# Optimization experiments

Hardware: AMD Instinct MI355X
Metric: run time of the kernel (lower is better)

Reference implementation:

```python
import jax, jax.numpy as jnp
import numpy as np

B, T, C = 4, 4096, 1024
H, CS = 16, 128
D = C // H
EPS = 1e-5

def _ln(x, g, b):
    m = jnp.mean(x, axis=-1, keepdims=True)
    v = jnp.var(x, axis=-1, keepdims=True)
    return (x - m) * jax.lax.rsqrt(v + EPS) * g + b

def setup_inputs() -> dict:
    key = jax.random.key(0)
    ks = jax.random.split(key, 12)
    s_c = 1.0 / np.sqrt(C)
    s_2d = 1.0 / np.sqrt(2 * D)
    return {
        "x": jax.random.normal(ks[0], (B, T, C), jnp.float32),
        "mark_W": jax.random.normal(ks[1], (C, C), jnp.float32) * s_c,
        "mark_b": jnp.zeros((C,), jnp.float32),
        "gate_W": jax.random.normal(ks[2], (C, C), jnp.float32) * s_c,
        "gate_b": jnp.zeros((C,), jnp.float32),
        "carry_g": jnp.ones((D,), jnp.float32),
        "carry_b": jnp.zeros((D,), jnp.float32),
        "card_g": jnp.ones((D,), jnp.float32),
        "card_b": jnp.zeros((D,), jnp.float32),
        "ho1_W": jax.random.normal(ks[3], (2 * D, 2 * D), jnp.float32) * s_2d,
        "ho1_b": jnp.zeros((2 * D,), jnp.float32),
        "ho2_W": jax.random.normal(ks[4], (2 * D, D), jnp.float32) * s_2d,
        "ho2_b": jnp.zeros((D,), jnp.float32),
        "proj_W": jax.random.normal(ks[5], (C, C), jnp.float32) * s_c * 0.02,
        "proj_b": jnp.zeros((C,), jnp.float32),
        "ln_g": jnp.ones((C,), jnp.float32),
        "ln_b": jnp.zeros((C,), jnp.float32),
    }

def reference(x, mark_W, mark_b, gate_W, gate_b, carry_g, carry_b,
              card_g, card_b, ho1_W, ho1_b, ho2_W, ho2_b,
              proj_W, proj_b, ln_g, ln_b):
    b, t, c = x.shape
    nc = t // CS  # T chosen divisible by chunk_size -> pad_len = 0
    pm = x @ mark_W + mark_b                       # [B,T,C]
    gates = jax.nn.sigmoid(x @ gate_W + gate_b)    # [B,T,C]

    def chunks(a):  # [B,T,C] -> [B,H,nc,CS,D]
        return a.reshape(b, nc, CS, H, D).transpose(0, 3, 1, 2, 4)

    x_h = chunks(x)
    gm = chunks(gates) * chunks(pm)                # gated marks
    lcm = jnp.cumsum(gm, axis=3)                   # local prefix sum within chunk
    chunk_sums = lcm[:, :, :, -1, :]               # [B,H,nc,D]
    carry_cum = jnp.cumsum(chunk_sums, axis=2)
    carries = jnp.concatenate(
        [jnp.zeros((b, H, 1, D), x.dtype), carry_cum[:, :, :-1, :]], axis=2)
    nrm_carry = _ln(carries, carry_g, carry_b)[:, :, :, None, :]  # [B,H,nc,1,D]
    mwc = lcm + nrm_carry                          # marks with carry
    cards_local = jnp.concatenate([nrm_carry, mwc[:, :, :, :-1, :]], axis=3)
    cards = _ln(cards_local, card_g, card_b)
    comb = jnp.concatenate([x_h, cards], axis=-1)  # [B,H,nc,CS,2D]
    h = jax.nn.gelu(comb @ ho1_W + ho1_b, approximate=False)
    ho = h @ ho2_W + ho2_b                         # [B,H,nc,CS,D]
    out = ho.transpose(0, 2, 3, 1, 4).reshape(b, t, c)
    out = out @ proj_W + proj_b
    out = _ln(out, ln_g, ln_b)
    return x + out
```

## Files before the change

### kernel.cpp

```cpp
#include <hip/hip_runtime.h>
#include <hip/hip_bf16.h>

typedef __bf16 bf16_t;
typedef __attribute__((ext_vector_type(8))) __bf16 bf16x8;
typedef __attribute__((ext_vector_type(4))) __bf16 bf16x4;
typedef __attribute__((ext_vector_type(4))) float f32x4;

static constexpr int Bn = 4, Tn = 4096, Cn = 1024, Hn = 16, CSn = 128, Dn = 64, NCn = 32;

#define DEVINL __device__ __forceinline__

DEVINL float wsum64(float v) {
  v += __shfl_xor(v, 32, 64);
  v += __shfl_xor(v, 16, 64);
  v += __shfl_xor(v, 8, 64);
  v += __shfl_xor(v, 4, 64);
  v += __shfl_xor(v, 2, 64);
  v += __shfl_xor(v, 1, 64);
  return v;
}

DEVINL float gelu_f(float v) {
  float x = v * 0.70710678f;
  float ax = fabsf(x);
  float t = 1.f / (1.f + 0.3275911f * ax);
  float poly = t * (0.254829592f +
               t * (-0.284496736f +
               t * (1.421413741f +
               t * (-1.453152027f +
               t * 1.061405429f))));
  float e = __expf(-ax * ax);
  float erfax = 1.f - poly * e;
  float erfx = copysignf(erfax, x);
  return 0.5f * v * (1.f + erfx);
}

DEVINL void gld16(const bf16_t* g, bf16_t* l) {
  __builtin_amdgcn_global_load_lds(
      (const __attribute__((address_space(1))) unsigned int*)(g),
      (__attribute__((address_space(3))) unsigned int*)(l), 16, 0, 0);
}

__global__ __launch_bounds__(256) void k_xbf(const float* __restrict__ in,
                                             bf16_t* __restrict__ out) {
  int i = blockIdx.x * 256 + threadIdx.x;
  float4 a = *reinterpret_cast<const float4*>(in + (size_t)i * 8);
  float4 b = *reinterpret_cast<const float4*>(in + (size_t)i * 8 + 4);
  bf16x8 o = {(bf16_t)a.x, (bf16_t)a.y, (bf16_t)a.z, (bf16_t)a.w,
              (bf16_t)b.x, (bf16_t)b.y, (bf16_t)b.z, (bf16_t)b.w};
  *reinterpret_cast<bf16x8*>(out + (size_t)i * 8) = o;
}

__global__ void k_transpose(const float* __restrict__ in, bf16_t* __restrict__ out,
                            int rows, int cols) {
  __shared__ float tile[64][65];
  int c0 = blockIdx.x * 64, r0 = blockIdx.y * 64;
  int tx = threadIdx.x & 63, ty = threadIdx.x >> 6;
#pragma unroll
  for (int i = ty; i < 64; i += 4)
    tile[i][tx] = in[(size_t)(r0 + i) * cols + c0 + tx];
  __syncthreads();
#pragma unroll
  for (int i = ty; i < 64; i += 4)
    out[(size_t)(c0 + i) * rows + r0 + tx] = (bf16_t)tile[tx][i];
}

__global__ __launch_bounds__(256, 3) void k_dualgemm_gm(
    const bf16_t* __restrict__ X, const bf16_t* __restrict__ Wtm,
    const bf16_t* __restrict__ Wtg, const float* __restrict__ bm,
    const float* __restrict__ bg, bf16_t* __restrict__ lcm,
    float* __restrict__ csum) {
  constexpr int K = Cn, N = Cn;
  constexpr int GP = 68;
  __shared__ __align__(16) bf16_t L[16384];
  __shared__ float tot[4][64];
  int tid = threadIdx.x;
  int Lb = blockIdx.x;
  int xcd = Lb & 7, jj = Lb >> 3;
  int nb = jj & 15, mb = xcd + 8 * (jj >> 4);
  int m0 = mb * 128, n0 = nb * 64;
  int wave = tid >> 6, lane = tid & 63;
  int wm = wave >> 1, wn = wave & 1;
  int lr = lane & 15, lk = lane >> 4;
  int rl = lane >> 2;
  int cl = (lane & 3) * 8;
  f32x4 accP[4][2] = {};
  f32x4 accG[4][2] = {};

  const bf16_t* Xb = X + (size_t)m0 * K;
  const bf16_t* Wmb = Wtm + (size_t)n0 * K;
  const bf16_t* Wgb = Wtg + (size_t)n0 * K;
  bf16_t* LA = L;
  bf16_t* LBm = L + 8192;
  bf16_t* LBg = L + 12288;

#define STAGE3(buf, kt)                                                    \
  {                                                                        \
    _Pragma("unroll")                                                      \
    for (int c = 0; c < 2; ++c) {                                          \
      int ch = wave * 2 + c;                                               \
      gld16(Xb + (size_t)(ch * 16 + rl) * K + (kt) * 32 + cl,              \
            LA + (buf) * 4096 + ch * 512);                                 \
    }                                                                      \
    size_t gob = (size_t)(wave * 16 + rl) * K + (kt) * 32 + cl;            \
    gld16(Wmb + gob, LBm + (buf) * 2048 + wave * 512);                     \
    gld16(Wgb + gob, LBg + (buf) * 2048 + wave * 512);                     \
  }

  STAGE3(0, 0);
  __syncthreads();
  int cur = 0;
  for (int kt = 0; kt < 32; ++kt) {
    if (kt < 31) STAGE3(cur ^ 1, kt + 1);
    bf16x8 af[4], bmf[2], bgf[2];
#pragma unroll
    for (int i = 0; i < 4; ++i)
      af[i] = *reinterpret_cast<const bf16x8*>(
          &LA[cur * 4096 + (wm * 64 + i * 16 + lr) * 32 + lk * 8]);
#pragma unroll
    for (int j = 0; j < 2; ++j) {
      bmf[j] = *reinterpret_cast<const bf16x8*>(
          &LBm[cur * 2048 + (wn * 32 + j * 16 + lr) * 32 + lk * 8]);
      bgf[j] = *reinterpret_cast<const bf16x8*>(
          &LBg[cur * 2048 + (wn * 32 + j * 16 + lr) * 32 + lk * 8]);
    }
#pragma unroll
    for (int i = 0; i < 4; ++i)
#pragma unroll
      for (int j = 0; j < 2; ++j) {
        accP[i][j] = __builtin_amdgcn_mfma_f32_16x16x32_bf16(af[i], bmf[j], accP[i][j], 0, 0, 0);
        accG[i][j] = __builtin_amdgcn_mfma_f32_16x16x32_bf16(af[i], bgf[j], accG[i][j], 0, 0, 0);
      }
    __syncthreads();
    cur ^= 1;
  }
#undef STAGE3

  bf16_t* G = L;
#pragma unroll
  for (int j = 0; j < 2; ++j) {
    int col = wn * 32 + j * 16 + lr;
    float bmv = bm[n0 + col], bgv = bg[n0 + col];
#pragma unroll
    for (int i = 0; i < 4; ++i) {
      int rbase = wm * 64 + i * 16 + lk * 4;
#pragma unroll
      for (int r = 0; r < 4; ++r) {
        float p = accP[i][j][r] + bmv;
        float g = accG[i][j][r] + bgv;
        float s = 1.f / (1.f + __expf(-g));
        G[(rbase + r) * GP + col] = (bf16_t)(s * p);
      }
    }
  }
  __syncthreads();
  {
    int col = tid & 63;
    int q = tid >> 6;
    float lsum = 0.f;
#pragma unroll 8
    for (int r = 0; r < 32; ++r)
      lsum += (float)G[(q * 32 + r) * GP + col];
    tot[q][col] = lsum;
    __syncthreads();
    float run = 0.f;
#pragma unroll
    for (int qq = 0; qq < 3; ++qq)
      if (qq < q) run += tot[qq][col];
    int gc = n0 + col;
    size_t obase = (size_t)(m0 + q * 32) * N + gc;
#pragma unroll 8
    for (int r = 0; r < 32; ++r) {
      run += (float)G[(q * 32 + r) * GP + col];
      lcm[obase + (size_t)r * N] = (bf16_t)run;
    }
    if (q == 3) {
      int bb = m0 >> 12;
      int ci = (m0 >> 7) & 31;
      csum[(((size_t)bb * Hn + (gc >> 6)) * NCn + ci) * 64 + (gc & 63)] = run;
    }
  }
}

__global__ __launch_bounds__(256) void k_cards(
    const bf16_t* __restrict__ lcm, const float* __restrict__ csum,
    const float* __restrict__ crg, const float* __restrict__ crb,
    const float* __restrict__ cg, const float* __restrict__ cb,
    bf16_t* __restrict__ cards) {
  int blk = blockIdx.x;
  int ci = blk & 31, bh = blk >> 5;
  int h = bh & 15, b = bh >> 4;
  int wave = threadIdx.x >> 6, lane = threadIdx.x & 63;
  int lg = lane >> 3;
  int le = lane & 7;
  int d0 = le * 8;
  size_t xrow0 = (size_t)(b * Tn + ci * CSn);

  float cv[8] = {0.f, 0.f, 0.f, 0.f, 0.f, 0.f, 0.f, 0.f};
  for (int k = 0; k < ci; ++k) {
    const float* cp = csum + ((size_t)bh * NCn + k) * 64 + d0;
    float4 a = *reinterpret_cast<const float4*>(cp);
    float4 c = *reinterpret_cast<const float4*>(cp + 4);
    cv[0] += a.x; cv[1] += a.y; cv[2] += a.z; cv[3] += a.w;
    cv[4] += c.x; cv[5] += c.y; cv[6] += c.z; cv[7] += c.w;
  }
  float ncv[8], ggv[8], bbv[8];
  {
    float s = 0.f;
#pragma unroll
    for (int e = 0; e < 8; ++e) s += cv[e];
    s += __shfl_xor(s, 1, 64);
    s += __shfl_xor(s, 2, 64);
    s += __shfl_xor(s, 4, 64);
    float mean = s * (1.f / 64.f);
    float q = 0.f;
#pragma unroll
    for (int e = 0; e < 8; ++e) { float dv = cv[e] - mean; q += dv * dv; }
    q += __shfl_xor(q, 1, 64);
    q += __shfl_xor(q, 2, 64);
    q += __shfl_xor(q, 4, 64);
    float rs = rsqrtf(q * (1.f / 64.f) + 1e-5f);
#pragma unroll
    for (int e = 0; e < 8; ++e) {
      ncv[e] = (cv[e] - mean) * rs * crg[d0 + e] + crb[d0 + e];
      ggv[e] = cg[d0 + e];
      bbv[e] = cb[d0 + e];
    }
  }
#pragma unroll
  for (int it = 0; it < 4; ++it) {
    int pr = wave * 32 + it * 8 + lg;
    float v[8];
    if (pr > 0) {
      bf16x8 lv = *reinterpret_cast<const bf16x8*>(
          lcm + (xrow0 + pr - 1) * Cn + h * Dn + d0);
#pragma unroll
      for (int e = 0; e < 8; ++e) v[e] = (float)lv[e] + ncv[e];
    } else {
#pragma unroll
      for (int e = 0; e < 8; ++e) v[e] = ncv[e];
    }
    float s = 0.f;
#pragma unroll
    for (int e = 0; e < 8; ++e) s += v[e];
    s += __shfl_xor(s, 1, 64);
    s += __shfl_xor(s, 2, 64);
    s += __shfl_xor(s, 4, 64);
    float mean = s * (1.f / 64.f);
    float q = 0.f;
#pragma unroll
    for (int e = 0; e < 8; ++e) { float dv = v[e] - mean; q += dv * dv; }
    q += __shfl_xor(q, 1, 64);
    q += __shfl_xor(q, 2, 64);
    q += __shfl_xor(q, 4, 64);
    float rs = rsqrtf(q * (1.f / 64.f) + 1e-5f);
    bf16x8 o;
#pragma unroll
    for (int e = 0; e < 8; ++e)
      o[e] = (bf16_t)((v[e] - mean) * rs * ggv[e] + bbv[e]);
    *reinterpret_cast<bf16x8*>(cards + ((size_t)blk * CSn + pr) * 64 + d0) = o;
  }
}

__global__ __launch_bounds__(256, 3) void k_ho_fused(
    const bf16_t* __restrict__ X, const bf16_t* __restrict__ cards,
    const bf16_t* __restrict__ W1t, const float* __restrict__ b1,
    const bf16_t* __restrict__ W2t, const float* __restrict__ b2,
    bf16_t* __restrict__ ho) {
  __shared__ __align__(16) bf16_t S[128 * 136];
  int tid = threadIdx.x;
  int blk = blockIdx.x;
  int ci = blk & 31, bh = blk >> 5;
  int h = bh & 15, b = bh >> 4;
  int wave = tid >> 6, lane = tid & 63;
  int wm = wave >> 1, wn = wave & 1;
  int lr = lane & 15, lk = lane >> 4;
  size_t xrow0 = (size_t)(b * Tn + ci * CSn);

  bf16x8 af[4][4];
#pragma unroll
  for (int i = 0; i < 4; ++i) {
    const bf16_t* xr = X + (xrow0 + wm * 64 + i * 16 + lr) * Cn + h * Dn + lk * 8;
    af[0][i] = *reinterpret_cast<const bf16x8*>(xr);
    af[1][i] = *reinterpret_cast<const bf16x8*>(xr + 32);
    const bf16_t* cr = cards + ((size_t)blk * CSn + wm * 64 + i * 16 + lr) * 64 + lk * 8;
    af[2][i] = *reinterpret_cast<const bf16x8*>(cr);
    af[3][i] = *reinterpret_cast<const bf16x8*>(cr + 32);
  }

  f32x4 acc[4][4] = {};
#pragma unroll
  for (int ks = 0; ks < 4; ++ks) {
    bf16x8 bfr[4];
#pragma unroll
    for (int j = 0; j < 4; ++j)
      bfr[j] = *reinterpret_cast<const bf16x8*>(
          W1t + (size_t)(wn * 64 + j * 16 + lr) * 128 + ks * 32 + lk * 8);
#pragma unroll
    for (int i = 0; i < 4; ++i)
#pragma unroll
      for (int j = 0; j < 4; ++j)
        acc[i][j] = __builtin_amdgcn_mfma_f32_16x16x32_bf16(af[ks][i], bfr[j], acc[i][j], 0, 0, 0);
  }
#pragma unroll
  for (int j = 0; j < 4; ++j) {
    int col = wn * 64 + j * 16 + lr;
    float bv = b1[col];
#pragma unroll
    for (int i = 0; i < 4; ++i) {
      int rbase = wm * 64 + i * 16 + lk * 4;
#pragma unroll
      for (int r = 0; r < 4; ++r)
        S[(rbase + r) * 136 + col] = (bf16_t)gelu_f(acc[i][j][r] + bv);
    }
  }
  __syncthreads();
  f32x4 acc2[2][4] = {};
#pragma unroll
  for (int ks = 0; ks < 4; ++ks) {
    bf16x8 ha[2], bfr[4];
#pragma unroll
    for (int i = 0; i < 2; ++i)
      ha[i] = *reinterpret_cast<const bf16x8*>(
          &S[(wave * 32 + i * 16 + lr) * 136 + ks * 32 + lk * 8]);
#pragma unroll
    for (int j = 0; j < 4; ++j)
      bfr[j] = *reinterpret_cast<const bf16x8*>(
          W2t + (size_t)(j * 16 + lr) * 128 + ks * 32 + lk * 8);
#pragma unroll
    for (int i = 0; i < 2; ++i)
#pragma unroll
      for (int j = 0; j < 4; ++j)
        acc2[i][j] = __builtin_amdgcn_mfma_f32_16x16x32_bf16(ha[i], bfr[j], acc2[i][j], 0, 0, 0);
  }
#pragma unroll
  for (int j = 0; j < 4; ++j) {
    int dd = j * 16 + lr;
    float bv = b2[dd];
#pragma unroll
    for (int i = 0; i < 2; ++i) {
      int pbase = wave * 32 + i * 16 + lk * 4;
#pragma unroll
      for (int r = 0; r < 4; ++r)
        ho[(xrow0 + pbase + r) * Cn + h * Dn + dd] = (bf16_t)(acc2[i][j][r] + bv);
    }
  }
}

__global__ __launch_bounds__(256, 3) void k_gemm_bt(
    const bf16_t* __restrict__ A, const bf16_t* __restrict__ Wt,
    const float* __restrict__ bias, bf16_t* __restrict__ out) {
  constexpr int K = Cn, N = Cn;
  __shared__ __align__(16) bf16_t L[4][128 * 32];
  int tid = threadIdx.x;
  int Lb = blockIdx.x + 8 * blockIdx.y;
  int xcd = Lb & 7, jj = Lb >> 3;
  int nb = jj & 7, mb = xcd + 8 * (jj >> 3);
  int m0 = mb * 128, n0 = nb * 128;
  int wave = tid >> 6, lane = tid & 63;
  int wm = wave >> 1, wn = wave & 1;
  int lr = lane & 15, lk = lane >> 4;
  int rl = lane >> 2, cl = (lane & 3) * 8;
  f32x4 acc[4][4] = {};
  const bf16_t* Ab = A + (size_t)m0 * K;
  const bf16_t* Wb = Wt + (size_t)n0 * K;

#define STAGE2(buf, kt)                                                    \
  {                                                                        \
    _Pragma("unroll")                                                      \
    for (int c = 0; c < 2; ++c) {                                          \
      int ch = wave * 2 + c;                                               \
      size_t go = (size_t)(ch * 16 + rl) * K + (kt) * 32 + cl;             \
      int lo = ch * 512;                                                   \
      gld16(Ab + go, &L[0 + (buf)][lo]);                                   \
      gld16(Wb + go, &L[2 + (buf)][lo]);                                   \
    }                                                                      \
  }

  STAGE2(0, 0);
  __syncthreads();
  int cur = 0;
  for (int kt = 0; kt < 32; ++kt) {
    if (kt < 31) STAGE2(cur ^ 1, kt + 1);
    bf16x8 af[4], bfr[4];
#pragma unroll
    for (int i = 0; i < 4; ++i)
      af[i] = *reinterpret_cast<const bf16x8*>(&L[0 + cur][(wm * 64 + i * 16 + lr) * 32 + lk * 8]);
#pragma unroll
    for (int j = 0; j < 4; ++j)
      bfr[j] = *reinterpret_cast<const bf16x8*>(&L[2 + cur][(wn * 64 + j * 16 + lr) * 32 + lk * 8]);
#pragma unroll
    for (int i = 0; i < 4; ++i)
#pragma unroll
      for (int j = 0; j < 4; ++j)
        acc[i][j] = __builtin_amdgcn_mfma_f32_16x16x32_bf16(af[i], bfr[j], acc[i][j], 0, 0, 0);
    __syncthreads();
    cur ^= 1;
  }
#undef STAGE2
#pragma unroll
  for (int j = 0; j < 4; ++j) {
    int col = n0 + wn * 64 + j * 16 + lr;
    float bv = bias[col];
#pragma unroll
    for (int i = 0; i < 4; ++i) {
      int rbase = m0 + wm * 64 + i * 16 + lk * 4;
#pragma unroll
      for (int r = 0; r < 4; ++r)
        out[(size_t)(rbase + r) * N + col] = (bf16_t)(acc[i][j][r] + bv);
    }
  }
}

__global__ __launch_bounds__(256) void k_ln_residual(
    const bf16_t* __restrict__ pre, const bf16_t* __restrict__ Xb,
    const float* __restrict__ g, const float* __restrict__ be,
    float* __restrict__ out) {
  int row = blockIdx.x, t = threadIdx.x;
  size_t base = (size_t)row * Cn + t * 4;
  bf16x4 pv4 = *reinterpret_cast<const bf16x4*>(pre + base);
  float v0 = (float)pv4[0], v1 = (float)pv4[1], v2 = (float)pv4[2], v3 = (float)pv4[3];
  float s = v0 + v1 + v2 + v3;
  float q = v0 * v0 + v1 * v1 + v2 * v2 + v3 * v3;
  s = wsum64(s);
  q = wsum64(q);
  __shared__ float red[8];
  int wv = t >> 6, ln = t & 63;
  if (ln == 0) { red[wv] = s; red[4 + wv] = q; }
  __syncthreads();
  float tot = red[0] + red[1] + red[2] + red[3];
  float totq = red[4] + red[5] + red[6] + red[7];
  float mean = tot * (1.f / 1024.f);
  float var = totq * (1.f / 1024.f) - mean * mean;
  float rs = rsqrtf(fmaxf(var, 0.f) + 1e-5f);
  bf16x4 xv4 = *reinterpret_cast<const bf16x4*>(Xb + base);
  float4 gv = *reinterpret_cast<const float4*>(g + t * 4);
  float4 bv = *reinterpret_cast<const float4*>(be + t * 4);
  float4 o;
  o.x = (v0 - mean) * rs * gv.x + bv.x + (float)xv4[0];
  o.y = (v1 - mean) * rs * gv.y + bv.y + (float)xv4[1];
  o.z = (v2 - mean) * rs * gv.z + bv.z + (float)xv4[2];
  o.w = (v3 - mean) * rs * gv.w + bv.w + (float)xv4[3];
  *reinterpret_cast<float4*>(out + base) = o;
}

extern "C" void kernel_launch(void* const* d_in, const int* in_sizes, int n_in,
                              void* d_out, int out_size, void* d_ws, size_t ws_size,
                              hipStream_t stream) {
  const float* x       = (const float*)d_in[0];
  const float* mark_W  = (const float*)d_in[1];
  const float* mark_b  = (const float*)d_in[2];
  const float* gate_W  = (const float*)d_in[3];
  const float* gate_b  = (const float*)d_in[4];
  const float* carry_g = (const float*)d_in[5];
  const float* carry_b = (const float*)d_in[6];
  const float* card_g  = (const float*)d_in[7];
  const float* card_b  = (const float*)d_in[8];
  const float* ho1_W   = (const float*)d_in[9];
  const float* ho1_b   = (const float*)d_in[10];
  const float* ho2_W   = (const float*)d_in[11];
  const float* ho2_b   = (const float*)d_in[12];
  const float* proj_W  = (const float*)d_in[13];
  const float* proj_b  = (const float*)d_in[14];
  const float* ln_g    = (const float*)d_in[15];
  const float* ln_b    = (const float*)d_in[16];
  float* out = (float*)d_out;

  char* ws = (char*)d_ws;
  bf16_t* xbf    = (bf16_t*)(ws + 0);
  bf16_t* gm     = (bf16_t*)(ws + 33554432);
  bf16_t* cards  = (bf16_t*)(ws + 67108864);
  bf16_t* outpre = (bf16_t*)(ws + 67108864);
  bf16_t* hobuf  = (bf16_t*)(ws + 100663296);
  float*  csum   = (float*)(ws + 134217728);
  bf16_t* wtm    = (bf16_t*)(ws + 135266304);
  bf16_t* wtg    = (bf16_t*)(ws + 137363456);
  bf16_t* wtp    = (bf16_t*)(ws + 139460608);
  bf16_t* wt1    = (bf16_t*)(ws + 141557760);
  bf16_t* wt2    = (bf16_t*)(ws + 141590528);

  k_xbf<<<8192, 256, 0, stream>>>(x, xbf);
  k_transpose<<<dim3(16, 16), 256, 0, stream>>>(mark_W, wtm, 1024, 1024);
  k_transpose<<<dim3(16, 16), 256, 0, stream>>>(gate_W, wtg, 1024, 1024);
  k_transpose<<<dim3(16, 16), 256, 0, stream>>>(proj_W, wtp, 1024, 1024);
  k_transpose<<<dim3(2, 2),   256, 0, stream>>>(ho1_W, wt1, 128, 128);
  k_transpose<<<dim3(1, 2),   256, 0, stream>>>(ho2_W, wt2, 128, 64);

  k_dualgemm_gm<<<2048, 256, 0, stream>>>(xbf, wtm, wtg, mark_b, gate_b, gm, csum);
  k_cards<<<2048, 256, 0, stream>>>(gm, csum, carry_g, carry_b, card_g, card_b, cards);
  k_ho_fused<<<2048, 256, 0, stream>>>(xbf, cards, wt1, ho1_b, wt2, ho2_b, hobuf);
  k_gemm_bt<<<dim3(8, 128), 256, 0, stream>>>(hobuf, wtp, proj_b, outpre);
  k_ln_residual<<<16384, 256, 0, stream>>>(outpre, xbf, ln_g, ln_b, out);
}
```

Measured before the change: 278.7 us.

## Double K-tile to 64 with XOR-swizzled LDS in GEMMs; stage cards via LDS

The two main GEMM kernels now load 64-wide K tiles per stage instead of 32. This halves the number of barrier-separated iterations. An XOR swizzle on the 16-byte column index avoids LDS bank conflicts on the wider rows. The cost is double the LDS footprint, so the launch-bounds occupancy hint drops from 3 to 2. The fused head-output kernel now stages its cards operand through swizzled LDS with direct-to-LDS loads instead of per-lane global vector loads, and its occupancy hint rises to 4. The extra barriers in that kernel add some synchronisation.

```diff
diff --git a/kernel.cpp b/kernel.cpp
--- a/kernel.cpp
+++ b/kernel.cpp
@@ -65,14 +65,14 @@
     out[(size_t)(c0 + i) * rows + r0 + tx] = (bf16_t)tile[tx][i];
 }
 
-__global__ __launch_bounds__(256, 3) void k_dualgemm_gm(
+__global__ __launch_bounds__(256, 2) void k_dualgemm_gm(
     const bf16_t* __restrict__ X, const bf16_t* __restrict__ Wtm,
     const bf16_t* __restrict__ Wtg, const float* __restrict__ bm,
     const float* __restrict__ bg, bf16_t* __restrict__ lcm,
     float* __restrict__ csum) {
   constexpr int K = Cn, N = Cn;
   constexpr int GP = 68;
-  __shared__ __align__(16) bf16_t L[16384];
+  __shared__ __align__(16) bf16_t L[32768];
   __shared__ float tot[4][64];
   int tid = threadIdx.x;
   int Lb = blockIdx.x;
@@ -82,8 +82,8 @@
   int wave = tid >> 6, lane = tid & 63;
   int wm = wave >> 1, wn = wave & 1;
   int lr = lane & 15, lk = lane >> 4;
-  int rl = lane >> 2;
-  int cl = (lane & 3) * 8;
+  int sr = lane >> 3;
+  int sc = (lane & 7) ^ sr;
   f32x4 accP[4][2] = {};
   f32x4 accG[4][2] = {};
 
@@ -91,46 +91,54 @@
   const bf16_t* Wmb = Wtm + (size_t)n0 * K;
   const bf16_t* Wgb = Wtg + (size_t)n0 * K;
   bf16_t* LA = L;
-  bf16_t* LBm = L + 8192;
-  bf16_t* LBg = L + 12288;
+  bf16_t* LBm = L + 16384;
+  bf16_t* LBg = L + 24576;
 
 #define STAGE3(buf, kt)                                                    \
   {                                                                        \
     _Pragma("unroll")                                                      \
+    for (int c = 0; c < 4; ++c) {                                          \
+      int r8 = wave * 32 + c * 8;                                          \
+      gld16(Xb + (size_t)(r8 + sr) * K + (kt) * 64 + sc * 8,               \
+            LA + (buf) * 8192 + r8 * 64);                                  \
+    }                                                                      \
+    _Pragma("unroll")                                                      \
     for (int c = 0; c < 2; ++c) {                                          \
-      int ch = wave * 2 + c;                                               \
-      gld16(Xb + (size_t)(ch * 16 + rl) * K + (kt) * 32 + cl,              \
-            LA + (buf) * 4096 + ch * 512);                                 \
+      int r8 = wave * 16 + c * 8;                                          \
+      size_t go = (size_t)(r8 + sr) * K + (kt) * 64 + sc * 8;              \
+      gld16(Wmb + go, LBm + (buf) * 4096 + r8 * 64);                       \
+      gld16(Wgb + go, LBg + (buf) * 4096 + r8 * 64);                       \
     }                                                                      \
-    size_t gob = (size_t)(wave * 16 + rl) * K + (kt) * 32 + cl;            \
-    gld16(Wmb + gob, LBm + (buf) * 2048 + wave * 512);                     \
-    gld16(Wgb + gob, LBg + (buf) * 2048 + wave * 512);                     \
   }
 
   STAGE3(0, 0);
   __syncthreads();
   int cur = 0;
-  for (int kt = 0; kt < 32; ++kt) {
-    if (kt < 31) STAGE3(cur ^ 1, kt + 1);
-    bf16x8 af[4], bmf[2], bgf[2];
-#pragma unroll
-    for (int i = 0; i < 4; ++i)
-      af[i] = *reinterpret_cast<const bf16x8*>(
-          &LA[cur * 4096 + (wm * 64 + i * 16 + lr) * 32 + lk * 8]);
-#pragma unroll
-    for (int j = 0; j < 2; ++j) {
-      bmf[j] = *reinterpret_cast<const bf16x8*>(
-          &LBm[cur * 2048 + (wn * 32 + j * 16 + lr) * 32 + lk * 8]);
-      bgf[j] = *reinterpret_cast<const bf16x8*>(
-          &LBg[cur * 2048 + (wn * 32 + j * 16 + lr) * 32 + lk * 8]);
-    }
-#pragma unroll
-    for (int i = 0; i < 4; ++i)
+  for (int kt = 0; kt < 16; ++kt) {
+    if (kt < 15) STAGE3(cur ^ 1, kt + 1);
+#pragma unroll
+    for (int ks = 0; ks < 2; ++ks) {
+      int sl = ((ks * 4 + lk) ^ (lr & 7)) * 8;
+      bf16x8 af[4], bmf[2], bgf[2];
+#pragma unroll
+      for (int i = 0; i < 4; ++i)
+        af[i] = *reinterpret_cast<const bf16x8*>(
+            &LA[cur * 8192 + (wm * 64 + i * 16 + lr) * 64 + sl]);
 #pragma unroll
       for (int j = 0; j < 2; ++j) {
-        accP[i][j] = __builtin_amdgcn_mfma_f32_16x16x32_bf16(af[i], bmf[j], accP[i][j], 0, 0, 0);
-        accG[i][j] = __builtin_amdgcn_mfma_f32_16x16x32_bf16(af[i], bgf[j], accG[i][j], 0, 0, 0);
+        bmf[j] = *reinterpret_cast<const bf16x8*>(
+            &LBm[cur * 4096 + (wn * 32 + j * 16 + lr) * 64 + sl]);
+        bgf[j] = *reinterpret_cast<const bf16x8*>(
+            &LBg[cur * 4096 + (wn * 32 + j * 16 + lr) * 64 + sl]);
       }
+#pragma unroll
+      for (int i = 0; i < 4; ++i)
+#pragma unroll
+        for (int j = 0; j < 2; ++j) {
+          accP[i][j] = __builtin_amdgcn_mfma_f32_16x16x32_bf16(af[i], bmf[j], accP[i][j], 0, 0, 0);
+          accG[i][j] = __builtin_amdgcn_mfma_f32_16x16x32_bf16(af[i], bgf[j], accG[i][j], 0, 0, 0);
+        }
+    }
     __syncthreads();
     cur ^= 1;
   }
@@ -262,7 +270,7 @@
   }
 }
 
-__global__ __launch_bounds__(256, 3) void k_ho_fused(
+__global__ __launch_bounds__(256, 4) void k_ho_fused(
     const bf16_t* __restrict__ X, const bf16_t* __restrict__ cards,
     const bf16_t* __restrict__ W1t, const float* __restrict__ b1,
     const bf16_t* __restrict__ W2t, const float* __restrict__ b2,
@@ -277,21 +285,38 @@
   int lr = lane & 15, lk = lane >> 4;
   size_t xrow0 = (size_t)(b * Tn + ci * CSn);
 
-  bf16x8 af[4][4];
+  {
+    const bf16_t* cbase = cards + (size_t)blk * CSn * 64;
+#pragma unroll
+    for (int c = 0; c < 4; ++c) {
+      int row = wave * 32 + c * 8 + (lane >> 3);
+      int c16 = (lane & 7) ^ (row & 7);
+      gld16(cbase + (size_t)row * 64 + c16 * 8, S + (wave * 32 + c * 8) * 64);
+    }
+  }
+  bf16x8 xf0[4], xf1[4];
 #pragma unroll
   for (int i = 0; i < 4; ++i) {
     const bf16_t* xr = X + (xrow0 + wm * 64 + i * 16 + lr) * Cn + h * Dn + lk * 8;
-    af[0][i] = *reinterpret_cast<const bf16x8*>(xr);
-    af[1][i] = *reinterpret_cast<const bf16x8*>(xr + 32);
-    const bf16_t* cr = cards + ((size_t)blk * CSn + wm * 64 + i * 16 + lr) * 64 + lk * 8;
-    af[2][i] = *reinterpret_cast<const bf16x8*>(cr);
-    af[3][i] = *reinterpret_cast<const bf16x8*>(cr + 32);
-  }
+    xf0[i] = *reinterpret_cast<const bf16x8*>(xr);
+    xf1[i] = *reinterpret_cast<const bf16x8*>(xr + 32);
+  }
+  __syncthreads();
 
   f32x4 acc[4][4] = {};
 #pragma unroll
   for (int ks = 0; ks < 4; ++ks) {
-    bf16x8 bfr[4];
+    bf16x8 af[4], bfr[4];
+#pragma unroll
+    for (int i = 0; i < 4; ++i) {
+      if (ks == 0)      af[i] = xf0[i];
+      else if (ks == 1) af[i] = xf1[i];
+      else {
+        int row = wm * 64 + i * 16 + lr;
+        int c16 = ((ks - 2) * 4 + lk) ^ (lr & 7);
+        af[i] = *reinterpret_cast<const bf16x8*>(&S[row * 64 + c16 * 8]);
+      }
+    }
 #pragma unroll
     for (int j = 0; j < 4; ++j)
       bfr[j] = *reinterpret_cast<const bf16x8*>(
@@ -300,8 +325,9 @@
     for (int i = 0; i < 4; ++i)
 #pragma unroll
       for (int j = 0; j < 4; ++j)
-        acc[i][j] = __builtin_amdgcn_mfma_f32_16x16x32_bf16(af[ks][i], bfr[j], acc[i][j], 0, 0, 0);
-  }
+        acc[i][j] = __builtin_amdgcn_mfma_f32_16x16x32_bf16(af[i], bfr[j], acc[i][j], 0, 0, 0);
+  }
+  __syncthreads();
 #pragma unroll
   for (int j = 0; j < 4; ++j) {
     int col = wn * 64 + j * 16 + lr;
@@ -318,10 +344,10 @@
   f32x4 acc2[2][4] = {};
 #pragma unroll
   for (int ks = 0; ks < 4; ++ks) {
-    bf16x8 ha[2], bfr[4];
+    bf16x8 af[2], bfr[4];
 #pragma unroll
     for (int i = 0; i < 2; ++i)
-      ha[i] = *reinterpret_cast<const bf16x8*>(
+      af[i] = *reinterpret_cast<const bf16x8*>(
           &S[(wave * 32 + i * 16 + lr) * 136 + ks * 32 + lk * 8]);
 #pragma unroll
     for (int j = 0; j < 4; ++j)
@@ -331,7 +357,7 @@
     for (int i = 0; i < 2; ++i)
 #pragma unroll
       for (int j = 0; j < 4; ++j)
-        acc2[i][j] = __builtin_amdgcn_mfma_f32_16x16x32_bf16(ha[i], bfr[j], acc2[i][j], 0, 0, 0);
+        acc2[i][j] = __builtin_amdgcn_mfma_f32_16x16x32_bf16(af[i], bfr[j], acc2[i][j], 0, 0, 0);
   }
 #pragma unroll
   for (int j = 0; j < 4; ++j) {
@@ -347,11 +373,11 @@
   }
 }
 
-__global__ __launch_bounds__(256, 3) void k_gemm_bt(
+__global__ __launch_bounds__(256, 2) void k_gemm_bt(
     const bf16_t* __restrict__ A, const bf16_t* __restrict__ Wt,
     const float* __restrict__ bias, bf16_t* __restrict__ out) {
   constexpr int K = Cn, N = Cn;
-  __shared__ __align__(16) bf16_t L[4][128 * 32];
+  __shared__ __align__(16) bf16_t L[32768];
   int tid = threadIdx.x;
   int Lb = blockIdx.x + 8 * blockIdx.y;
   int xcd = Lb & 7, jj = Lb >> 3;
@@ -360,40 +386,48 @@
   int wave = tid >> 6, lane = tid & 63;
   int wm = wave >> 1, wn = wave & 1;
   int lr = lane & 15, lk = lane >> 4;
-  int rl = lane >> 2, cl = (lane & 3) * 8;
+  int sr = lane >> 3;
+  int sc = (lane & 7) ^ sr;
   f32x4 acc[4][4] = {};
   const bf16_t* Ab = A + (size_t)m0 * K;
   const bf16_t* Wb = Wt + (size_t)n0 * K;
+  bf16_t* LA = L;
+  bf16_t* LB = L + 16384;
 
 #define STAGE2(buf, kt)                                                    \
   {                                                                        \
     _Pragma("unroll")                                                      \
-    for (int c = 0; c < 2; ++c) {                                          \
-      int ch = wave * 2 + c;                                               \
-      size_t go = (size_t)(ch * 16 + rl) * K + (kt) * 32 + cl;             \
-      int lo = ch * 512;                                                   \
-      gld16(Ab + go, &L[0 + (buf)][lo]);                                   \
-      gld16(Wb + go, &L[2 + (buf)][lo]);                                   \
+    for (int c = 0; c < 4; ++c) {                                          \
+      int r8 = wave * 32 + c * 8;                                          \
+      size_t go = (size_t)(r8 + sr) * K + (kt) * 64 + sc * 8;              \
+      gld16(Ab + go, LA + (buf) * 8192 + r8 * 64);                         \
+      gld16(Wb + go, LB + (buf) * 8192 + r8 * 64);                         \
     }                                                                      \
   }
 
   STAGE2(0, 0);
   __syncthreads();
   int cur = 0;
-  for (int kt = 0; kt < 32; ++kt) {
-    if (kt < 31) STAGE2(cur ^ 1, kt + 1);
-    bf16x8 af[4], bfr[4];
-#pragma unroll
-    for (int i = 0; i < 4; ++i)
-      af[i] = *reinterpret_cast<const bf16x8*>(&L[0 + cur][(wm * 64 + i * 16 + lr) * 32 + lk * 8]);
-#pragma unroll
-    for (int j = 0; j < 4; ++j)
-      bfr[j] = *reinterpret_cast<const bf16x8*>(&L[2 + cur][(wn * 64 + j * 16 + lr) * 32 + lk * 8]);
-#pragma unroll
-    for (int i = 0; i < 4; ++i)
+  for (int kt = 0; kt < 16; ++kt) {
+    if (kt < 15) STAGE2(cur ^ 1, kt + 1);
+#pragma unroll
+    for (int ks = 0; ks < 2; ++ks) {
+      int sl = ((ks * 4 + lk) ^ (lr & 7)) * 8;
+      bf16x8 af[4], bfr[4];
+#pragma unroll
+      for (int i = 0; i < 4; ++i)
+        af[i] = *reinterpret_cast<const bf16x8*>(
+            &LA[cur * 8192 + (wm * 64 + i * 16 + lr) * 64 + sl]);
 #pragma unroll
       for (int j = 0; j < 4; ++j)
-        acc[i][j] = __builtin_amdgcn_mfma_f32_16x16x32_bf16(af[i], bfr[j], acc[i][j], 0, 0, 0);
+        bfr[j] = *reinterpret_cast<const bf16x8*>(
+            &LB[cur * 8192 + (wn * 64 + j * 16 + lr) * 64 + sl]);
+#pragma unroll
+      for (int i = 0; i < 4; ++i)
+#pragma unroll
+        for (int j = 0; j < 4; ++j)
+          acc[i][j] = __builtin_amdgcn_mfma_f32_16x16x32_bf16(af[i], bfr[j], acc[i][j], 0, 0, 0);
+    }
     __syncthreads();
     cur ^= 1;
   }
```

New measurement: 265.8 us. 1.05x faster.
